# Kernel optimization log

Measured on AMD Instinct MI355X. Metric: run time of the kernel, lower is better.

## Reference

```python
import jax, jax.numpy as jnp
import numpy as np

N_HEAD = 16
D_K = 64
D_V = 64
EMBED = 1024
BATCH = 4
SEQ = 2048

def setup_inputs() -> dict:
    key = jax.random.key(0)
    ks = jax.random.split(key, 12)
    s = lambda d: 1.0 / np.sqrt(d)
    u = lambda k, shape, d: jax.random.uniform(k, shape, jnp.float32, -s(d), s(d))
    return {
        'z': jax.random.normal(ks[0], (BATCH, SEQ, EMBED), jnp.float32),
        'wq': u(ks[1], (EMBED, D_K), D_K),
        'wk': u(ks[2], (EMBED, D_K), D_K),
        'wv': u(ks[3], (EMBED, D_V), D_V),
        'fcq_w': u(ks[4], (D_K, N_HEAD * D_K), D_K),
        'fcq_b': u(ks[5], (N_HEAD * D_K,), N_HEAD * D_K),
        'fck_w': u(ks[6], (D_K, N_HEAD * D_K), D_K),
        'fck_b': u(ks[7], (N_HEAD * D_K,), N_HEAD * D_K),
        'fcv_w': u(ks[8], (D_V, N_HEAD * D_V), D_V),
        'fcv_b': u(ks[9], (N_HEAD * D_V,), N_HEAD * D_V),
        'fco_w': u(ks[10], (N_HEAD * D_V, EMBED), EMBED),
        'fco_b': u(ks[11], (EMBED,), EMBED),
    }

def reference(z, wq, wk, wv, fcq_w, fcq_b, fck_w, fck_b, fcv_w, fcv_b, fco_w, fco_b):
    b, n, _ = z.shape
    scale = jnp.sqrt(jnp.float32(D_K))
    # bottleneck projections then per-head expansion
    q = (z @ wq) @ fcq_w + fcq_b  # [b, n, H*dk]
    k = (z @ wk) @ fck_w + fck_b  # [b, n, H*dk]
    v = (z @ wv) @ fcv_w + fcv_b  # [b, n, H*dv]
    q = q.reshape(b, n, N_HEAD, D_K)
    k = k.reshape(b, n, N_HEAD, D_K)
    v = v.reshape(b, n, N_HEAD, D_V)
    scores = jnp.einsum('bihd,bjhd->bhij', q, k) / scale  # [b, H, n, n]
    attn = jax.nn.softmax(scores, axis=-1)
    out = jnp.einsum('bhij,bjhd->bihd', attn, v)  # [b, n, H, dv]
    out = out.reshape(b, n, N_HEAD * D_V)
    return out @ fco_w + fco_b  # [b, n, embed]
```

## Files before the change

kernel.cpp:

```cpp
#include <hip/hip_runtime.h>


typedef __bf16 bf16x8 __attribute__((ext_vector_type(8)));
typedef __bf16 bf16x4 __attribute__((ext_vector_type(4)));
typedef __bf16 bf16x2 __attribute__((ext_vector_type(2)));
typedef float floatx4 __attribute__((ext_vector_type(4)));
typedef float floatx16 __attribute__((ext_vector_type(16)));
typedef unsigned int uintx4 __attribute__((ext_vector_type(4)));
typedef unsigned int uintx2 __attribute__((ext_vector_type(2)));

#define LDP 72

#define SW64(row, col) (((row) << 6) | (((((col) >> 3) ^ ((row) & 7) ^ (((row) >> 3) & 7)) << 3) | ((col) & 7)))

#if __has_builtin(__builtin_amdgcn_exp2f)
__device__ __forceinline__ float fast_exp2(float x) { return __builtin_amdgcn_exp2f(x); }
#else
__device__ __forceinline__ float fast_exp2(float x) { return exp2f(x); }
#endif

__device__ __forceinline__ unsigned int pack_bf16(float lo, float hi) {
    bf16x2 w; w[0] = (__bf16)lo; w[1] = (__bf16)hi;
    return __builtin_bit_cast(unsigned int, w);
}
__device__ __forceinline__ unsigned int pack2(__bf16 lo, __bf16 hi) {
    bf16x2 w; w[0] = lo; w[1] = hi;
    return __builtin_bit_cast(unsigned int, w);
}
#if __has_builtin(__builtin_amdgcn_permlane32_swap)
__device__ __forceinline__ void xchg(unsigned int& X, unsigned int& Y, int) {
    uintx2 r = __builtin_amdgcn_permlane32_swap(X, Y, false, false);
    X = r[0]; Y = r[1];
}
#else
__device__ __forceinline__ void xchg(unsigned int& X, unsigned int& Y, int hl) {
    unsigned int sX = (unsigned int)__shfl_xor((int)X, 32);
    unsigned int sY = (unsigned int)__shfl_xor((int)Y, 32);
    unsigned int lo = hl ? sY : X;
    unsigned int hi = hl ? Y : sX;
    X = lo; Y = hi;
}
#endif
__device__ __forceinline__ bf16x8 frag4(unsigned int a, unsigned int b, unsigned int c, unsigned int d) {
    uintx4 u; u[0] = a; u[1] = b; u[2] = c; u[3] = d;
    return __builtin_bit_cast(bf16x8, u);
}
__device__ __forceinline__ void async_b128(const __bf16* g, __bf16* l) {
    __builtin_amdgcn_global_load_lds(
        (const __attribute__((address_space(1))) unsigned int*)g,
        (__attribute__((address_space(3))) unsigned int*)l, 16, 0, 0);
}

__global__ void detect_dtype(const unsigned short* __restrict__ z, int* __restrict__ flag) {
    __shared__ int cnt;
    if (threadIdx.x == 0) cnt = 0;
    __syncthreads();
    int local = 0;
    for (int i = threadIdx.x; i < 16384; i += 256) {
        unsigned int u = (unsigned int)z[i] << 16;
        float x = __uint_as_float(u);
        float ax = fabsf(x);
        if (!(ax <= 1024.0f) || (x != 0.0f && ax < 1e-20f)) local++;
    }
    atomicAdd(&cnt, local);
    __syncthreads();
    if (threadIdx.x == 0) *flag = (cnt > 1310) ? 1 : 0;
}

struct ConvArgs { const void* src[12]; int n[12]; int off[12]; };

__global__ void convert_inputs(ConvArgs a, __bf16* __restrict__ cv, const int* __restrict__ flag,
                               int base_k) {
    const int k = blockIdx.y + base_k;
    const int i = (blockIdx.x * 256 + threadIdx.x) * 8;
    if (i >= a.n[k]) return;
    __bf16* dst = cv + a.off[k] + i;
    if (*flag) {
        const float* s = (const float*)a.src[k] + i;
        float4 f0 = *(const float4*)s;
        float4 f1 = *(const float4*)(s + 4);
        bf16x8 v;
        v[0] = (__bf16)f0.x; v[1] = (__bf16)f0.y; v[2] = (__bf16)f0.z; v[3] = (__bf16)f0.w;
        v[4] = (__bf16)f1.x; v[5] = (__bf16)f1.y; v[6] = (__bf16)f1.z; v[7] = (__bf16)f1.w;
        *(bf16x8*)dst = v;
    } else {
        *(bf16x8*)dst = *(const bf16x8*)((const __bf16*)a.src[k] + i);
    }
}

__global__ __launch_bounds__(256) void transpose_w(
    const __bf16* __restrict__ in, __bf16* __restrict__ out, int K,
    int zsin, int zsout)
{
    in  += blockIdx.z * zsin;
    out += blockIdx.z * zsout;
    __shared__ __bf16 t[64][72];
    const int bn = blockIdx.x * 64, bk = blockIdx.y * 64;
    const int r = threadIdx.x >> 3, c8 = (threadIdx.x & 7) << 3;
    #pragma unroll
    for (int p = 0; p < 2; p++) {
        bf16x8 v = *(const bf16x8*)&in[(bk + p * 32 + r) * 1024 + bn + c8];
        #pragma unroll
        for (int j = 0; j < 8; j++) t[c8 + j][p * 32 + r] = v[j];
    }
    __syncthreads();
    #pragma unroll
    for (int p = 0; p < 2; p++) {
        bf16x8 v;
        #pragma unroll
        for (int j = 0; j < 8; j++) v[j] = t[p * 32 + r][c8 + j];
        *(bf16x8*)&out[(bn + p * 32 + r) * K + bk + c8] = v;
    }
}

__global__ __launch_bounds__(256) void gemm_bias(
    const __bf16* __restrict__ A0, const __bf16* __restrict__ A1, const __bf16* __restrict__ A2,
    const __bf16* __restrict__ B0, const __bf16* __restrict__ B1, const __bf16* __restrict__ B2,
    const __bf16* __restrict__ bias0, const __bf16* __restrict__ bias1, const __bf16* __restrict__ bias2,
    void* __restrict__ C0, void* __restrict__ C1, void* __restrict__ C2,
    int M, int N, int K, int has_bias, const int* flagp,
    float os0, float os1, float os2)
{
    const int zsel = blockIdx.z;
    const __bf16* A = (zsel == 0) ? A0 : (zsel == 1) ? A1 : A2;
    const __bf16* B = (zsel == 0) ? B0 : (zsel == 1) ? B1 : B2;
    const __bf16* bias = (zsel == 0) ? bias0 : (zsel == 1) ? bias1 : bias2;
    void* C = (zsel == 0) ? C0 : (zsel == 1) ? C1 : C2;
    const float oscale = (zsel == 0) ? os0 : (zsel == 1) ? os1 : os2;
    const int out_fp32 = flagp ? *flagp : 0;

    const int m0 = blockIdx.x * 128;
    const int n0 = blockIdx.y * 64;
    const int tid = threadIdx.x;
    const int wave = tid >> 6;
    const int ln = tid & 15;
    const int quad = (tid >> 4) & 3;

    __shared__ __bf16 As[128 * LDP];
    __shared__ __bf16 Bts[64 * 64];

    floatx4 acc[2][4] = {};

    for (int k0 = 0; k0 < K; k0 += 64) {
        __syncthreads();
        for (int i = tid; i < 1024; i += 256) {
            int r = i >> 3, c8 = (i & 7) << 3;
            *(bf16x8*)&As[r * LDP + c8] = *(const bf16x8*)&A[(m0 + r) * K + k0 + c8];
        }
        for (int i = tid; i < 512; i += 256) {
            int kk = i >> 3, a8 = (i & 7) << 3;
            bf16x8 v = *(const bf16x8*)&B[(k0 + kk) * N + n0 + a8];
            #pragma unroll
            for (int j = 0; j < 8; j++) Bts[SW64(a8 + j, kk)] = v[j];
        }
        __syncthreads();
        #pragma unroll
        for (int ks = 0; ks < 2; ks++) {
            bf16x8 a[2], b[4];
            a[0] = *(const bf16x8*)&As[(wave * 32 + ln) * LDP + ks * 32 + quad * 8];
            a[1] = *(const bf16x8*)&As[(wave * 32 + 16 + ln) * LDP + ks * 32 + quad * 8];
            #pragma unroll
            for (int nt = 0; nt < 4; nt++)
                b[nt] = *(const bf16x8*)&Bts[SW64(nt * 16 + ln, ks * 32 + quad * 8)];
            #pragma unroll
            for (int rt = 0; rt < 2; rt++)
                #pragma unroll
                for (int nt = 0; nt < 4; nt++)
                    acc[rt][nt] = __builtin_amdgcn_mfma_f32_16x16x32_bf16(a[rt], b[nt], acc[rt][nt], 0, 0, 0);
        }
    }
    #pragma unroll
    for (int rt = 0; rt < 2; rt++) {
        const int row = m0 + wave * 32 + rt * 16 + quad * 4;
        #pragma unroll
        for (int nt = 0; nt < 4; nt++) {
            const int col = n0 + nt * 16 + ln;
            float bv = has_bias ? (float)bias[col] : 0.0f;
            #pragma unroll
            for (int r = 0; r < 4; r++) {
                float val = (acc[rt][nt][r] + bv) * oscale;
                if (out_fp32) ((float*)C)[(row + r) * N + col] = val;
                else ((__bf16*)C)[(row + r) * N + col] = (__bf16)val;
            }
        }
    }
}

__global__ __launch_bounds__(256, 2) void gemm128(
    const __bf16* __restrict__ A0, const __bf16* __restrict__ A1, const __bf16* __restrict__ A2,
    const __bf16* __restrict__ BT0, const __bf16* __restrict__ BT1, const __bf16* __restrict__ BT2,
    const __bf16* __restrict__ bias0, const __bf16* __restrict__ bias1, const __bf16* __restrict__ bias2,
    void* __restrict__ C0, void* __restrict__ C1, void* __restrict__ C2,
    int M, int N, int K, const int* flagp,
    float os0, float os1, float os2)
{
    const int zsel = blockIdx.z;
    const __bf16* A = (zsel == 0) ? A0 : (zsel == 1) ? A1 : A2;
    const __bf16* BT = (zsel == 0) ? BT0 : (zsel == 1) ? BT1 : BT2;
    const __bf16* bias = (zsel == 0) ? bias0 : (zsel == 1) ? bias1 : bias2;
    void* C = (zsel == 0) ? C0 : (zsel == 1) ? C1 : C2;
    const float oscale = (zsel == 0) ? os0 : (zsel == 1) ? os1 : os2;
    const int out_fp32 = flagp ? *flagp : 0;

    const int m0 = blockIdx.x * 128;
    const int n0 = blockIdx.y * 128;
    const int tid = threadIdx.x;
    const int wave = tid >> 6, ln = tid & 63;
    const int wr = wave >> 1, wc = wave & 1;
    const int l15 = tid & 15, quad = (tid >> 4) & 3;

    __shared__ __bf16 As[128 * 64];
    __shared__ __bf16 Bs[128 * 64];

    const int r_off = ln >> 3, j_off = ln & 7;

    floatx4 acc[4][4] = {};

    for (int k0 = 0; k0 < K; k0 += 64) {
        __syncthreads();
        #pragma unroll
        for (int it = 0; it < 4; it++) {
            const int seg = wave * 4 + it;
            const int row = seg * 8 + r_off;
            const int c = j_off ^ (row & 7) ^ ((row >> 3) & 7);
            async_b128(&A[(m0 + row) * K + k0 + c * 8], &As[seg * 512]);
            async_b128(&BT[(n0 + row) * K + k0 + c * 8], &Bs[seg * 512]);
        }
        __syncthreads();
        #pragma unroll
        for (int ks = 0; ks < 2; ks++) {
            bf16x8 a[4], b[4];
            #pragma unroll
            for (int rt = 0; rt < 4; rt++)
                a[rt] = *(const bf16x8*)&As[SW64(wr * 64 + rt * 16 + l15, ks * 32 + quad * 8)];
            #pragma unroll
            for (int nt = 0; nt < 4; nt++)
                b[nt] = *(const bf16x8*)&Bs[SW64(wc * 64 + nt * 16 + l15, ks * 32 + quad * 8)];
            #pragma unroll
            for (int rt = 0; rt < 4; rt++)
                #pragma unroll
                for (int nt = 0; nt < 4; nt++)
                    acc[rt][nt] = __builtin_amdgcn_mfma_f32_16x16x32_bf16(a[rt], b[nt], acc[rt][nt], 0, 0, 0);
        }
    }
    #pragma unroll
    for (int rt = 0; rt < 4; rt++) {
        const int row = m0 + wr * 64 + rt * 16 + quad * 4;
        #pragma unroll
        for (int nt = 0; nt < 4; nt++) {
            const int col = n0 + wc * 64 + nt * 16 + l15;
            float bv = (float)bias[col];
            #pragma unroll
            for (int r = 0; r < 4; r++) {
                float val = (acc[rt][nt][r] + bv) * oscale;
                if (out_fp32) ((float*)C)[(row + r) * N + col] = val;
                else ((__bf16*)C)[(row + r) * N + col] = (__bf16)val;
            }
        }
    }
}

__global__ __launch_bounds__(256, 3) void attn_kernel(
    const __bf16* __restrict__ Qg, const __bf16* __restrict__ Kg,
    const __bf16* __restrict__ Vg, __bf16* __restrict__ Og)
{
    const int bh = blockIdx.x;
    const int b = bh >> 4, h = bh & 15;
    const int q0 = blockIdx.y * 128;
    const int base = b * 2048 * 1024 + h * 64;
    const int tid = threadIdx.x;
    const int wave = tid >> 6, ln = tid & 63;
    const int l31 = ln & 31, hl = ln >> 5;
    const int h8 = hl * 8;

    __shared__ __bf16 Ks[2][64 * 64];
    __shared__ __bf16 VTs[2][64 * 64];

    bf16x8 qf[4];
    #pragma unroll
    for (int ks = 0; ks < 4; ks++)
        qf[ks] = *(const bf16x8*)&Qg[base + (q0 + wave * 32 + l31) * 1024 + ks * 16 + h8];

    const int kr = tid >> 3, kc = (tid & 7) << 3;
    const int vr2 = (tid >> 3) * 2, vc = (tid & 7) << 3;

    {
        bf16x8 ka = *(const bf16x8*)&Kg[base + kr * 1024 + kc];
        bf16x8 kb = *(const bf16x8*)&Kg[base + (kr + 32) * 1024 + kc];
        bf16x8 va = *(const bf16x8*)&Vg[base + vr2 * 1024 + vc];
        bf16x8 vb = *(const bf16x8*)&Vg[base + (vr2 + 1) * 1024 + vc];
        *(bf16x8*)&Ks[0][SW64(kr, kc)] = ka;
        *(bf16x8*)&Ks[0][SW64(kr + 32, kc)] = kb;
        #pragma unroll
        for (int j = 0; j < 8; j++)
            *(unsigned int*)&VTs[0][SW64(vc + j, vr2)] = pack2(va[j], vb[j]);
    }

    floatx16 o_acc[2] = {};
    float m_i = -1e30f, l_i = 0.0f;

    for (int t = 0; t < 32; t++) {
        const int cur = t & 1, nxt = cur ^ 1;
        bf16x8 nka, nkb, nva, nvb;
        if (t < 31) {
            const int kvn = (t + 1) * 64;
            nka = *(const bf16x8*)&Kg[base + (kvn + kr) * 1024 + kc];
            nkb = *(const bf16x8*)&Kg[base + (kvn + kr + 32) * 1024 + kc];
            nva = *(const bf16x8*)&Vg[base + (kvn + vr2) * 1024 + vc];
            nvb = *(const bf16x8*)&Vg[base + (kvn + vr2 + 1) * 1024 + vc];
        }
        __syncthreads();

        floatx16 sv[2] = {};
        #pragma unroll
        for (int ks = 0; ks < 4; ks++) {
            bf16x8 a0 = *(const bf16x8*)&Ks[cur][SW64(l31, ks * 16 + h8)];
            bf16x8 a1 = *(const bf16x8*)&Ks[cur][SW64(32 + l31, ks * 16 + h8)];
            sv[0] = __builtin_amdgcn_mfma_f32_32x32x16_bf16(a0, qf[ks], sv[0], 0, 0, 0);
            sv[1] = __builtin_amdgcn_mfma_f32_32x32x16_bf16(a1, qf[ks], sv[1], 0, 0, 0);
        }

        float m8[8];
        #pragma unroll
        for (int r = 0; r < 8; r++)
            m8[r] = fmaxf(fmaxf(sv[0][r], sv[0][r + 8]), fmaxf(sv[1][r], sv[1][r + 8]));
        float mx = fmaxf(fmaxf(fmaxf(m8[0], m8[4]), fmaxf(m8[1], m8[5])),
                         fmaxf(fmaxf(m8[2], m8[6]), fmaxf(m8[3], m8[7])));
        mx = fmaxf(mx, __shfl_xor(mx, 32));

        if (__any(mx > m_i + 8.0f)) {
            float m_new = fmaxf(m_i, mx);
            float alpha = fast_exp2(m_i - m_new);
            m_i = m_new;
            l_i *= alpha;
            #pragma unroll
            for (int dt = 0; dt < 2; dt++)
                #pragma unroll
                for (int r = 0; r < 16; r++) o_acc[dt][r] *= alpha;
        }

        float p0[16], p1[16];
        #pragma unroll
        for (int r = 0; r < 16; r++) p0[r] = fast_exp2(sv[0][r] - m_i);
        #pragma unroll
        for (int r = 0; r < 16; r++) p1[r] = fast_exp2(sv[1][r] - m_i);
        float rsA = 0.f, rsB = 0.f, rsC = 0.f, rsD = 0.f;
        #pragma unroll
        for (int r = 0; r < 16; r += 4) {
            rsA += p0[r]; rsB += p0[r + 1]; rsC += p0[r + 2]; rsD += p0[r + 3];
            rsA += p1[r]; rsB += p1[r + 1]; rsC += p1[r + 2]; rsD += p1[r + 3];
        }
        float rs = (rsA + rsB) + (rsC + rsD);
        rs += __shfl_xor(rs, 32);
        l_i += rs;

        bf16x8 pf0, pf1, pf2, pf3;
        {
            unsigned int A0 = pack_bf16(p0[0], p0[1]),  B0 = pack_bf16(p0[2], p0[3]);
            unsigned int C0 = pack_bf16(p0[4], p0[5]),  D0 = pack_bf16(p0[6], p0[7]);
            unsigned int A1 = pack_bf16(p0[8], p0[9]),  B1 = pack_bf16(p0[10], p0[11]);
            unsigned int C1 = pack_bf16(p0[12], p0[13]), D1 = pack_bf16(p0[14], p0[15]);
            xchg(A0, C0, hl); xchg(B0, D0, hl); xchg(A1, C1, hl); xchg(B1, D1, hl);
            pf0 = frag4(A0, B0, C0, D0);
            pf1 = frag4(A1, B1, C1, D1);
        }
        {
            unsigned int A0 = pack_bf16(p1[0], p1[1]),  B0 = pack_bf16(p1[2], p1[3]);
            unsigned int C0 = pack_bf16(p1[4], p1[5]),  D0 = pack_bf16(p1[6], p1[7]);
            unsigned int A1 = pack_bf16(p1[8], p1[9]),  B1 = pack_bf16(p1[10], p1[11]);
            unsigned int C1 = pack_bf16(p1[12], p1[13]), D1 = pack_bf16(p1[14], p1[15]);
            xchg(A0, C0, hl); xchg(B0, D0, hl); xchg(A1, C1, hl); xchg(B1, D1, hl);
            pf2 = frag4(A0, B0, C0, D0);
            pf3 = frag4(A1, B1, C1, D1);
        }

        if (t < 31) {
            *(bf16x8*)&Ks[nxt][SW64(kr, kc)] = nka;
            *(bf16x8*)&Ks[nxt][SW64(kr + 32, kc)] = nkb;
        }

        #pragma unroll
        for (int js = 0; js < 4; js++) {
            bf16x8 av0 = *(const bf16x8*)&VTs[cur][SW64(l31, js * 16 + h8)];
            bf16x8 av1 = *(const bf16x8*)&VTs[cur][SW64(32 + l31, js * 16 + h8)];
            bf16x8 pb = (js == 0) ? pf0 : (js == 1) ? pf1 : (js == 2) ? pf2 : pf3;
            o_acc[0] = __builtin_amdgcn_mfma_f32_32x32x16_bf16(av0, pb, o_acc[0], 0, 0, 0);
            o_acc[1] = __builtin_amdgcn_mfma_f32_32x32x16_bf16(av1, pb, o_acc[1], 0, 0, 0);
        }

        if (t < 31) {
            #pragma unroll
            for (int j = 0; j < 8; j++)
                *(unsigned int*)&VTs[nxt][SW64(vc + j, vr2)] = pack2(nva[j], nvb[j]);
        }
    }

    float inv = 1.0f / l_i;
    const int orow = q0 + wave * 32 + l31;
    #pragma unroll
    for (int dt = 0; dt < 2; dt++)
        #pragma unroll
        for (int g = 0; g < 4; g++) {
            bf16x4 ov;
            #pragma unroll
            for (int e = 0; e < 4; e++) ov[e] = (__bf16)(o_acc[dt][g * 4 + e] * inv);
            *(bf16x4*)&Og[base + orow * 1024 + dt * 32 + g * 8 + hl * 4] = ov;
        }
}

extern "C" void kernel_launch(void* const* d_in, const int* in_sizes, int n_in,
                              void* d_out, int out_size, void* d_ws, size_t ws_size,
                              hipStream_t stream)
{
    int* flag = (int*)d_ws;
    __bf16* cv = (__bf16*)((char*)d_ws + 256);

    const int Z = 0, WQ = 8388608, WK = 8454144, WV = 8519680;
    const int FCQW = 8585216, FCKW = 8650752, FCVW = 8716288, FCOW = 8781824;
    const int FCQB = 9830400, FCKB = 9831424, FCVB = 9832448, FCOB = 9833472;
    __bf16* zb = cv + 10485760;
    __bf16* Qw = cv + 12582912;
    __bf16* Kw = Qw + 8388608;
    __bf16* Vw = Kw + 8388608;
    __bf16* Ow = cv + Z;
    __bf16* WT3 = cv + WQ;
    __bf16* OWT = zb;

    detect_dtype<<<1, 256, 0, stream>>>((const unsigned short*)d_in[0], flag);

    ConvArgs ca;
    const int offs[12] = {Z, WQ, WK, WV, FCQW, FCQB, FCKW, FCKB, FCVW, FCVB, FCOW, FCOB};
    for (int i = 0; i < 12; i++) { ca.src[i] = d_in[i]; ca.n[i] = in_sizes[i]; ca.off[i] = offs[i]; }
    convert_inputs<<<dim3(4096, 1), 256, 0, stream>>>(ca, cv, flag, 0);
    convert_inputs<<<dim3(512, 11), 256, 0, stream>>>(ca, cv, flag, 1);

    gemm_bias<<<dim3(64, 1, 3), 256, 0, stream>>>(
        cv + Z, cv + Z, cv + Z, cv + WQ, cv + WK, cv + WV,
        cv + FCQB, cv + FCQB, cv + FCQB,
        zb, zb + 524288, zb + 1048576, 8192, 64, 1024, 0, nullptr,
        1.0f, 1.0f, 1.0f);

    transpose_w<<<dim3(16, 1, 3), 256, 0, stream>>>(cv + FCQW, WT3, 64, 65536, 65536);

    const float QSC = 0.125f * 1.44269504088896f;
    gemm128<<<dim3(64, 8, 3), 256, 0, stream>>>(
        zb, zb + 524288, zb + 1048576,
        WT3, WT3 + 65536, WT3 + 131072,
        cv + FCQB, cv + FCKB, cv + FCVB,
        Qw, Kw, Vw, 8192, 1024, 64, nullptr,
        QSC, 1.0f, 1.0f);

    transpose_w<<<dim3(16, 16, 1), 256, 0, stream>>>(cv + FCOW, OWT, 1024, 0, 0);

    attn_kernel<<<dim3(64, 16), 256, 0, stream>>>(Qw, Kw, Vw, Ow);

    gemm128<<<dim3(64, 8, 1), 256, 0, stream>>>(
        Ow, Ow, Ow, OWT, OWT, OWT,
        cv + FCOB, cv + FCOB, cv + FCOB,
        d_out, d_out, d_out, 8192, 1024, 1024, flag,
        1.0f, 1.0f, 1.0f);
}
```

Baseline: 314.0 us.

## Fuse input conversion and weight transposes into one kernel; add async gemm64

Replaces the two convert launches and two transpose launches with a single mega_convert kernel that converts z and the biases and writes every weight matrix already transposed. The bottleneck projection is moved to a new gemm64 kernel that uses async global-to-LDS loads with swizzled layout, replacing the old gemm_bias with its scalar scattered B stores. This cuts launch count and extra memory passes over the weights. It also moves the FCO transposed weight to a dedicated buffer instead of reusing the zb scratch, and widens index arithmetic to long.

```diff
diff --git a/kernel.cpp b/kernel.cpp
--- a/kernel.cpp
+++ b/kernel.cpp
@@ -9,8 +9,6 @@
 typedef unsigned int uintx4 __attribute__((ext_vector_type(4)));
 typedef unsigned int uintx2 __attribute__((ext_vector_type(2)));
 
-#define LDP 72
-
 #define SW64(row, col) (((row) << 6) | (((((col) >> 3) ^ ((row) & 7) ^ (((row) >> 3) & 7)) << 3) | ((col) & 7)))
 
 #if __has_builtin(__builtin_amdgcn_exp2f)
@@ -49,6 +47,20 @@
     __builtin_amdgcn_global_load_lds(
         (const __attribute__((address_space(1))) unsigned int*)g,
         (__attribute__((address_space(3))) unsigned int*)l, 16, 0, 0);
+}
+
+__device__ __forceinline__ bf16x8 cvt8(const void* src, int f, long idx) {
+    bf16x8 v;
+    if (f) {
+        const float* s = (const float*)src + idx;
+        float4 f0 = *(const float4*)s;
+        float4 f1 = *(const float4*)(s + 4);
+        v[0] = (__bf16)f0.x; v[1] = (__bf16)f0.y; v[2] = (__bf16)f0.z; v[3] = (__bf16)f0.w;
+        v[4] = (__bf16)f1.x; v[5] = (__bf16)f1.y; v[6] = (__bf16)f1.z; v[7] = (__bf16)f1.w;
+    } else {
+        v = *(const bf16x8*)((const __bf16*)src + idx);
+    }
+    return v;
 }
 
 __global__ void detect_dtype(const unsigned short* __restrict__ z, int* __restrict__ flag) {
@@ -67,122 +79,105 @@
     if (threadIdx.x == 0) *flag = (cnt > 1310) ? 1 : 0;
 }
 
-struct ConvArgs { const void* src[12]; int n[12]; int off[12]; };
-
-__global__ void convert_inputs(ConvArgs a, __bf16* __restrict__ cv, const int* __restrict__ flag,
-                               int base_k) {
-    const int k = blockIdx.y + base_k;
-    const int i = (blockIdx.x * 256 + threadIdx.x) * 8;
-    if (i >= a.n[k]) return;
-    __bf16* dst = cv + a.off[k] + i;
-    if (*flag) {
-        const float* s = (const float*)a.src[k] + i;
-        float4 f0 = *(const float4*)s;
-        float4 f1 = *(const float4*)(s + 4);
-        bf16x8 v;
-        v[0] = (__bf16)f0.x; v[1] = (__bf16)f0.y; v[2] = (__bf16)f0.z; v[3] = (__bf16)f0.w;
-        v[4] = (__bf16)f1.x; v[5] = (__bf16)f1.y; v[6] = (__bf16)f1.z; v[7] = (__bf16)f1.w;
-        *(bf16x8*)dst = v;
+struct MegaArgs { const void* z; const void* bias[4]; const void* w[7]; };
+
+__global__ __launch_bounds__(256) void mega_convert(MegaArgs a, __bf16* __restrict__ cv,
+                                                    const int* __restrict__ flag) {
+    const int f = *flag;
+    const unsigned int blk = blockIdx.x;
+    const int tid = threadIdx.x;
+
+    if (blk < 4096) {
+        const long i = ((long)blk * 256 + tid) * 8;
+        *(bf16x8*)&cv[i] = cvt8(a.z, f, i);
+        return;
+    }
+    if (blk < 4098) {
+        const int idx = (((int)blk - 4096) * 256 + tid) * 8;
+        const int b = idx >> 10, o = idx & 1023;
+        *(bf16x8*)&cv[9830400 + b * 1024 + o] = cvt8(a.bias[b], f, o);
+        return;
+    }
+    const int t = blk - 4098;
+    int bx, by, R, C;
+    const void* src;
+    __bf16* dst;
+    if (t < 48) {
+        const int m = t >> 4; by = t & 15; bx = 0; R = 1024; C = 64;
+        src = a.w[m]; dst = cv + 8388608 + m * 65536;
+    } else if (t < 96) {
+        const int m = (t - 48) >> 4; bx = (t - 48) & 15; by = 0; R = 64; C = 1024;
+        src = a.w[3 + m]; dst = cv + 8585216 + m * 65536;
     } else {
-        *(bf16x8*)dst = *(const bf16x8*)((const __bf16*)a.src[k] + i);
-    }
-}
-
-__global__ __launch_bounds__(256) void transpose_w(
-    const __bf16* __restrict__ in, __bf16* __restrict__ out, int K,
-    int zsin, int zsout)
-{
-    in  += blockIdx.z * zsin;
-    out += blockIdx.z * zsout;
-    __shared__ __bf16 t[64][72];
-    const int bn = blockIdx.x * 64, bk = blockIdx.y * 64;
-    const int r = threadIdx.x >> 3, c8 = (threadIdx.x & 7) << 3;
+        const int u = t - 96; bx = u & 15; by = u >> 4; R = 1024; C = 1024;
+        src = a.w[6]; dst = cv + 8781824;
+    }
+    __shared__ __bf16 tl[64][72];
+    const int r0 = by * 64, c0 = bx * 64;
+    const int rr = tid >> 3, c8 = (tid & 7) << 3;
     #pragma unroll
     for (int p = 0; p < 2; p++) {
-        bf16x8 v = *(const bf16x8*)&in[(bk + p * 32 + r) * 1024 + bn + c8];
-        #pragma unroll
-        for (int j = 0; j < 8; j++) t[c8 + j][p * 32 + r] = v[j];
+        bf16x8 v = cvt8(src, f, (long)(r0 + p * 32 + rr) * C + c0 + c8);
+        #pragma unroll
+        for (int j = 0; j < 8; j++) tl[c8 + j][p * 32 + rr] = v[j];
     }
     __syncthreads();
     #pragma unroll
     for (int p = 0; p < 2; p++) {
         bf16x8 v;
         #pragma unroll
-        for (int j = 0; j < 8; j++) v[j] = t[p * 32 + r][c8 + j];
-        *(bf16x8*)&out[(bn + p * 32 + r) * K + bk + c8] = v;
-    }
-}
-
-__global__ __launch_bounds__(256) void gemm_bias(
-    const __bf16* __restrict__ A0, const __bf16* __restrict__ A1, const __bf16* __restrict__ A2,
-    const __bf16* __restrict__ B0, const __bf16* __restrict__ B1, const __bf16* __restrict__ B2,
-    const __bf16* __restrict__ bias0, const __bf16* __restrict__ bias1, const __bf16* __restrict__ bias2,
-    void* __restrict__ C0, void* __restrict__ C1, void* __restrict__ C2,
-    int M, int N, int K, int has_bias, const int* flagp,
-    float os0, float os1, float os2)
+        for (int j = 0; j < 8; j++) v[j] = tl[p * 32 + rr][c8 + j];
+        *(bf16x8*)&dst[(long)(c0 + p * 32 + rr) * R + r0 + c8] = v;
+    }
+}
+
+__global__ __launch_bounds__(256, 2) void gemm64(
+    const __bf16* __restrict__ A,
+    const __bf16* __restrict__ BT0, const __bf16* __restrict__ BT1, const __bf16* __restrict__ BT2,
+    __bf16* __restrict__ C0, __bf16* __restrict__ C1, __bf16* __restrict__ C2,
+    int K)
 {
     const int zsel = blockIdx.z;
-    const __bf16* A = (zsel == 0) ? A0 : (zsel == 1) ? A1 : A2;
-    const __bf16* B = (zsel == 0) ? B0 : (zsel == 1) ? B1 : B2;
-    const __bf16* bias = (zsel == 0) ? bias0 : (zsel == 1) ? bias1 : bias2;
-    void* C = (zsel == 0) ? C0 : (zsel == 1) ? C1 : C2;
-    const float oscale = (zsel == 0) ? os0 : (zsel == 1) ? os1 : os2;
-    const int out_fp32 = flagp ? *flagp : 0;
-
-    const int m0 = blockIdx.x * 128;
-    const int n0 = blockIdx.y * 64;
+    const __bf16* BT = (zsel == 0) ? BT0 : (zsel == 1) ? BT1 : BT2;
+    __bf16* C = (zsel == 0) ? C0 : (zsel == 1) ? C1 : C2;
+    const int m0 = blockIdx.x * 64;
     const int tid = threadIdx.x;
-    const int wave = tid >> 6;
-    const int ln = tid & 15;
-    const int quad = (tid >> 4) & 3;
-
-    __shared__ __bf16 As[128 * LDP];
-    __shared__ __bf16 Bts[64 * 64];
-
-    floatx4 acc[2][4] = {};
+    const int wave = tid >> 6, ln = tid & 63;
+    const int l15 = tid & 15, quad = (tid >> 4) & 3;
+
+    __shared__ __bf16 As[64 * 64];
+    __shared__ __bf16 Bs[64 * 64];
+
+    const int r_off = ln >> 3, j_off = ln & 7;
+    floatx4 acc[4] = {};
 
     for (int k0 = 0; k0 < K; k0 += 64) {
         __syncthreads();
-        for (int i = tid; i < 1024; i += 256) {
-            int r = i >> 3, c8 = (i & 7) << 3;
-            *(bf16x8*)&As[r * LDP + c8] = *(const bf16x8*)&A[(m0 + r) * K + k0 + c8];
-        }
-        for (int i = tid; i < 512; i += 256) {
-            int kk = i >> 3, a8 = (i & 7) << 3;
-            bf16x8 v = *(const bf16x8*)&B[(k0 + kk) * N + n0 + a8];
-            #pragma unroll
-            for (int j = 0; j < 8; j++) Bts[SW64(a8 + j, kk)] = v[j];
+        #pragma unroll
+        for (int it = 0; it < 2; it++) {
+            const int seg = wave * 2 + it;
+            const int row = seg * 8 + r_off;
+            const int c = j_off ^ (row & 7) ^ ((row >> 3) & 7);
+            async_b128(&A[(long)(m0 + row) * K + k0 + c * 8], &As[seg * 512]);
+            async_b128(&BT[(long)row * K + k0 + c * 8], &Bs[seg * 512]);
         }
         __syncthreads();
         #pragma unroll
         for (int ks = 0; ks < 2; ks++) {
-            bf16x8 a[2], b[4];
-            a[0] = *(const bf16x8*)&As[(wave * 32 + ln) * LDP + ks * 32 + quad * 8];
-            a[1] = *(const bf16x8*)&As[(wave * 32 + 16 + ln) * LDP + ks * 32 + quad * 8];
-            #pragma unroll
-            for (int nt = 0; nt < 4; nt++)
-                b[nt] = *(const bf16x8*)&Bts[SW64(nt * 16 + ln, ks * 32 + quad * 8)];
-            #pragma unroll
-            for (int rt = 0; rt < 2; rt++)
-                #pragma unroll
-                for (int nt = 0; nt < 4; nt++)
-                    acc[rt][nt] = __builtin_amdgcn_mfma_f32_16x16x32_bf16(a[rt], b[nt], acc[rt][nt], 0, 0, 0);
-        }
-    }
-    #pragma unroll
-    for (int rt = 0; rt < 2; rt++) {
-        const int row = m0 + wave * 32 + rt * 16 + quad * 4;
-        #pragma unroll
-        for (int nt = 0; nt < 4; nt++) {
-            const int col = n0 + nt * 16 + ln;
-            float bv = has_bias ? (float)bias[col] : 0.0f;
-            #pragma unroll
-            for (int r = 0; r < 4; r++) {
-                float val = (acc[rt][nt][r] + bv) * oscale;
-                if (out_fp32) ((float*)C)[(row + r) * N + col] = val;
-                else ((__bf16*)C)[(row + r) * N + col] = (__bf16)val;
+            bf16x8 av = *(const bf16x8*)&As[SW64(wave * 16 + l15, ks * 32 + quad * 8)];
+            #pragma unroll
+            for (int nt = 0; nt < 4; nt++) {
+                bf16x8 bv = *(const bf16x8*)&Bs[SW64(nt * 16 + l15, ks * 32 + quad * 8)];
+                acc[nt] = __builtin_amdgcn_mfma_f32_16x16x32_bf16(av, bv, acc[nt], 0, 0, 0);
             }
         }
+    }
+    #pragma unroll
+    for (int nt = 0; nt < 4; nt++) {
+        const int col = nt * 16 + l15;
+        #pragma unroll
+        for (int r = 0; r < 4; r++)
+            C[(long)(m0 + wave * 16 + quad * 4 + r) * 64 + col] = (__bf16)acc[nt][r];
     }
 }
 
@@ -223,8 +218,8 @@
             const int seg = wave * 4 + it;
             const int row = seg * 8 + r_off;
             const int c = j_off ^ (row & 7) ^ ((row >> 3) & 7);
-            async_b128(&A[(m0 + row) * K + k0 + c * 8], &As[seg * 512]);
-            async_b128(&BT[(n0 + row) * K + k0 + c * 8], &Bs[seg * 512]);
+            async_b128(&A[(long)(m0 + row) * K + k0 + c * 8], &As[seg * 512]);
+            async_b128(&BT[(long)(n0 + row) * K + k0 + c * 8], &Bs[seg * 512]);
         }
         __syncthreads();
         #pragma unroll
@@ -253,8 +248,8 @@
             #pragma unroll
             for (int r = 0; r < 4; r++) {
                 float val = (acc[rt][nt][r] + bv) * oscale;
-                if (out_fp32) ((float*)C)[(row + r) * N + col] = val;
-                else ((__bf16*)C)[(row + r) * N + col] = (__bf16)val;
+                if (out_fp32) ((float*)C)[(long)(row + r) * N + col] = val;
+                else ((__bf16*)C)[(long)(row + r) * N + col] = (__bf16)val;
             }
         }
     }
@@ -415,48 +410,40 @@
     int* flag = (int*)d_ws;
     __bf16* cv = (__bf16*)((char*)d_ws + 256);
 
-    const int Z = 0, WQ = 8388608, WK = 8454144, WV = 8519680;
-    const int FCQW = 8585216, FCKW = 8650752, FCVW = 8716288, FCOW = 8781824;
-    const int FCQB = 9830400, FCKB = 9831424, FCVB = 9832448, FCOB = 9833472;
+    const int Z = 0, WQT = 8388608, FCWT = 8585216, FCOWT = 8781824, BIAS = 9830400;
     __bf16* zb = cv + 10485760;
     __bf16* Qw = cv + 12582912;
     __bf16* Kw = Qw + 8388608;
     __bf16* Vw = Kw + 8388608;
     __bf16* Ow = cv + Z;
-    __bf16* WT3 = cv + WQ;
-    __bf16* OWT = zb;
 
     detect_dtype<<<1, 256, 0, stream>>>((const unsigned short*)d_in[0], flag);
 
-    ConvArgs ca;
-    const int offs[12] = {Z, WQ, WK, WV, FCQW, FCQB, FCKW, FCKB, FCVW, FCVB, FCOW, FCOB};
-    for (int i = 0; i < 12; i++) { ca.src[i] = d_in[i]; ca.n[i] = in_sizes[i]; ca.off[i] = offs[i]; }
-    convert_inputs<<<dim3(4096, 1), 256, 0, stream>>>(ca, cv, flag, 0);
-    convert_inputs<<<dim3(512, 11), 256, 0, stream>>>(ca, cv, flag, 1);
-
-    gemm_bias<<<dim3(64, 1, 3), 256, 0, stream>>>(
-        cv + Z, cv + Z, cv + Z, cv + WQ, cv + WK, cv + WV,
-        cv + FCQB, cv + FCQB, cv + FCQB,
-        zb, zb + 524288, zb + 1048576, 8192, 64, 1024, 0, nullptr,
-        1.0f, 1.0f, 1.0f);
-
-    transpose_w<<<dim3(16, 1, 3), 256, 0, stream>>>(cv + FCQW, WT3, 64, 65536, 65536);
+    MegaArgs ma;
+    ma.z = d_in[0];
+    ma.bias[0] = d_in[5]; ma.bias[1] = d_in[7]; ma.bias[2] = d_in[9]; ma.bias[3] = d_in[11];
+    ma.w[0] = d_in[1]; ma.w[1] = d_in[2]; ma.w[2] = d_in[3];
+    ma.w[3] = d_in[4]; ma.w[4] = d_in[6]; ma.w[5] = d_in[8];
+    ma.w[6] = d_in[10];
+    mega_convert<<<dim3(4450, 1), 256, 0, stream>>>(ma, cv, flag);
+
+    gemm64<<<dim3(128, 1, 3), 256, 0, stream>>>(
+        cv + Z, cv + WQT, cv + WQT + 65536, cv + WQT + 131072,
+        zb, zb + 524288, zb + 1048576, 1024);
 
     const float QSC = 0.125f * 1.44269504088896f;
     gemm128<<<dim3(64, 8, 3), 256, 0, stream>>>(
         zb, zb + 524288, zb + 1048576,
-        WT3, WT3 + 65536, WT3 + 131072,
-        cv + FCQB, cv + FCKB, cv + FCVB,
+        cv + FCWT, cv + FCWT + 65536, cv + FCWT + 131072,
+        cv + BIAS, cv + BIAS + 1024, cv + BIAS + 2048,
         Qw, Kw, Vw, 8192, 1024, 64, nullptr,
         QSC, 1.0f, 1.0f);
 
-    transpose_w<<<dim3(16, 16, 1), 256, 0, stream>>>(cv + FCOW, OWT, 1024, 0, 0);
-
     attn_kernel<<<dim3(64, 16), 256, 0, stream>>>(Qw, Kw, Vw, Ow);
 
     gemm128<<<dim3(64, 8, 1), 256, 0, stream>>>(
-        Ow, Ow, Ow, OWT, OWT, OWT,
-        cv + FCOB, cv + FCOB, cv + FCOB,
+        Ow, Ow, Ow, cv + FCOWT, cv + FCOWT, cv + FCOWT,
+        cv + BIAS + 3072, cv + BIAS + 3072, cv + BIAS + 3072,
         d_out, d_out, d_out, 8192, 1024, 1024, flag,
         1.0f, 1.0f, 1.0f);
 }
```

Measured after the change: 267.5 us. 1.17x faster.
